# Kernel optimization log

Hardware: AMD Instinct MI355X
Metric: run time of the kernel (lower is better)

The kernel has to match this reference:

```python
import jax, jax.numpy as jnp
import numpy as np

NEG_SLOPE = 0.2

def gat_conv(x, src, dst, W, a_src, a_dst, b, heads, out_ch, num_nodes):
    # Linear projection per head: [N, H, C]
    h = (x @ W).reshape(num_nodes, heads, out_ch)
    # Per-node attention logits: [N, H]
    s_src = jnp.sum(h * a_src[None, :, :], axis=-1)
    s_dst = jnp.sum(h * a_dst[None, :, :], axis=-1)
    # Per-edge attention score, LeakyReLU(0.2): [E, H]
    e = jax.nn.leaky_relu(s_src[src] + s_dst[dst], negative_slope=NEG_SLOPE)
    # Segment softmax over incoming edges of each destination node
    e_max = jax.ops.segment_max(e, dst, num_segments=num_nodes)
    e_exp = jnp.exp(e - e_max[dst])
    denom = jax.ops.segment_sum(e_exp, dst, num_segments=num_nodes)
    alpha = e_exp / (denom[dst] + 1e-16)  # [E, H]
    # Weighted message aggregation: [N, H, C]
    msg = h[src] * alpha[:, :, None]
    out = jax.ops.segment_sum(msg, dst, num_segments=num_nodes)
    # Concat heads + bias
    return out.reshape(num_nodes, heads * out_ch) + b


def setup_inputs() -> dict:
    key = jax.random.key(0)
    ks = jax.random.split(key, 9)
    N, E = 50000, 1000000
    x = jax.random.normal(ks[0], (N, 300), dtype=jnp.float32)
    edge_index = jax.random.randint(ks[1], (2, E), 0, N, dtype=jnp.int64)
    W1 = jax.random.normal(ks[2], (300, 64), dtype=jnp.float32) * 0.05
    a_src1 = jax.random.normal(ks[3], (8, 8), dtype=jnp.float32) * 0.1
    a_dst1 = jax.random.normal(ks[4], (8, 8), dtype=jnp.float32) * 0.1
    b1 = jnp.zeros((64,), dtype=jnp.float32)
    W2 = jax.random.normal(ks[5], (64, 64), dtype=jnp.float32) * 0.1
    a_src2 = jax.random.normal(ks[6], (1, 64), dtype=jnp.float32) * 0.1
    a_dst2 = jax.random.normal(ks[7], (1, 64), dtype=jnp.float32) * 0.1
    b2 = jnp.zeros((64,), dtype=jnp.float32)
    return {"x": x, "edge_index": edge_index, "W1": W1, "a_src1": a_src1,
            "a_dst1": a_dst1, "b1": b1, "W2": W2, "a_src2": a_src2,
            "a_dst2": a_dst2, "b2": b2}


def reference(x, edge_index, W1, a_src1, a_dst1, b1, W2, a_src2, a_dst2, b2):
    N = x.shape[0]
    src, dst = edge_index[0], edge_index[1]
    # eval mode: dropouts are identity
    h = gat_conv(x, src, dst, W1, a_src1, a_dst1, b1, heads=8, out_ch=8, num_nodes=N)
    h = jax.nn.elu(h)
    out = gat_conv(h, src, dst, W2, a_src2, a_dst2, b2, heads=1, out_ch=64, num_nodes=N)
    return out
```

## Files before the change

### kernel.cpp

```cpp
#include <hip/hip_runtime.h>
#include <math.h>

#define NN 50000
#define NE 1000000
#define EC 31
#define ECP 32
#define CSH 15
#define WR 8
#define RNG 6250
#define RPAD 6272
#define NCNT (EC * WR)
#define NPB 24
#define NGB 782
#define NSB 196

typedef __bf16 bf16x8 __attribute__((ext_vector_type(8)));
typedef float f32x4 __attribute__((ext_vector_type(4)));

__device__ inline unsigned short f2bf(float f) {
    unsigned u = __float_as_uint(f);
    u += 0x7FFFu + ((u >> 16) & 1u);
    return (unsigned short)(u >> 16);
}
__device__ inline float bf2f(unsigned short s) {
    return __uint_as_float(((unsigned)s) << 16);
}
__device__ inline float bflo(unsigned r) { return __uint_as_float(r << 16); }
__device__ inline float bfhi(unsigned r) { return __uint_as_float(r & 0xffff0000u); }
__device__ inline unsigned cvtpk(float lo, float hi) {
    unsigned u;
    asm("v_cvt_pk_bf16_f32 %0, %1, %2" : "=v"(u) : "v"(lo), "v"(hi));
    return u;
}

__global__ __launch_bounds__(1024) void k_count_prep(
        const int* __restrict__ ei, int* __restrict__ cnt,
        unsigned char* __restrict__ pos,
        const float* __restrict__ W1, const float* __restrict__ W2,
        unsigned short* __restrict__ Bt1, unsigned short* __restrict__ Bt2)
{
    __shared__ __align__(16) int sm[RNG];
    const int tid = threadIdx.x;
    const int bid = blockIdx.x;

    if (bid >= NCNT) {
        int t = (bid - NCNT) * 1024 + tid;
        if (t < 64 * 320) {
            int c = t / 320, k = t % 320;
            Bt1[t] = (k < 300) ? f2bf(W1[k * 64 + c]) : (unsigned short)0;
        } else {
            int i = t - 64 * 320;
            int c = i >> 6, k = i & 63;
            Bt2[i] = f2bf(W2[k * 64 + c]);
        }
        return;
    }
    const int c = bid >> 3, w = bid & 7;
    const int lo = w * RNG;
    for (int j = tid; j < RNG; j += 1024) sm[j] = 0;
    __syncthreads();
    const int base = c << CSH;
    #pragma unroll
    for (int it = 0; it < (1 << CSH) / 4096; ++it) {
        int e = base + (it * 1024 + tid) * 4;
        if (e < NE) {
            int4 d = *(const int4*)(ei + NE + e);
            unsigned t0 = (unsigned)(d.x - lo), t1 = (unsigned)(d.y - lo);
            unsigned t2 = (unsigned)(d.z - lo), t3 = (unsigned)(d.w - lo);
            if (t0 < RNG) pos[e]     = (unsigned char)atomicAdd(&sm[t0], 1);
            if (t1 < RNG) pos[e + 1] = (unsigned char)atomicAdd(&sm[t1], 1);
            if (t2 < RNG) pos[e + 2] = (unsigned char)atomicAdd(&sm[t2], 1);
            if (t3 < RNG) pos[e + 3] = (unsigned char)atomicAdd(&sm[t3], 1);
        }
    }
    __syncthreads();
    int* dstp = cnt + (size_t)bid * RPAD;
    for (int j = tid; j < RNG; j += 1024) dstp[j] = sm[j];
}

__global__ __launch_bounds__(256) void k_gemm_scan(
        const float* __restrict__ A, const unsigned short* __restrict__ Bt,
        unsigned short* __restrict__ hb,
        const float* __restrict__ asrc, const float* __restrict__ adst,
        float* __restrict__ ss, float* __restrict__ sd,
        const int* __restrict__ cnt, int* __restrict__ excl,
        int* __restrict__ sums, unsigned char* __restrict__ rpre)
{
    __shared__ __align__(16) unsigned short lds[9216];
    const int tid = threadIdx.x;
    const int bid = blockIdx.x;

    if (bid >= NGB) {
        const int sb = bid - NGB;
        int i = sb * 256 + tid;
        int v = 0;
        if (i < NN) {
            int w8 = i / RNG;
            int j = i - w8 * RNG;
            int run = 0;
            unsigned pk[ECP / 4];
            #pragma unroll
            for (int q = 0; q < ECP / 4; ++q) pk[q] = 0;
            #pragma unroll
            for (int cc = 0; cc < EC; ++cc) {
                pk[cc >> 2] |= ((unsigned)run & 0xffu) << ((cc & 3) * 8);
                run += cnt[(size_t)(cc * 8 + w8) * RPAD + j];
            }
            v = run;
            *(uint4*)(rpre + (size_t)i * ECP)      = make_uint4(pk[0], pk[1], pk[2], pk[3]);
            *(uint4*)(rpre + (size_t)i * ECP + 16) = make_uint4(pk[4], pk[5], pk[6], pk[7]);
        }
        int* buf = (int*)lds;
        buf[tid] = v;
        __syncthreads();
        #pragma unroll
        for (int off = 1; off < 256; off <<= 1) {
            int t = (tid >= off) ? buf[tid - off] : 0;
            __syncthreads();
            buf[tid] += t;
            __syncthreads();
        }
        if (i < NN) excl[i] = buf[tid] - v;
        if (tid == 255) sums[sb] = buf[255];
        return;
    }

    const int row0 = bid * 64;
    const int lane = tid & 63, w = tid >> 6;
    const int quad = lane >> 4, mm = lane & 15;
    const int sr = tid >> 2, q16 = (tid & 3) * 16;
    const int gsr = row0 + sr;
    const int K = 300, M = NN;

    f32x4 acc[4];
    #pragma unroll
    for (int i = 0; i < 4; ++i) acc[i] = (f32x4){0.f, 0.f, 0.f, 0.f};

    for (int kt = 0; kt < 5; ++kt) {
        const int k0 = kt * 64;
        int4 a0 = {0, 0, 0, 0}, a1 = {0, 0, 0, 0};
        if (gsr < M) {
            const float* ap = A + (size_t)gsr * K + k0 + q16;
            if (k0 + q16 + 15 < K) {
                float4 v0 = *(const float4*)ap;
                float4 v1 = *(const float4*)(ap + 4);
                float4 v2 = *(const float4*)(ap + 8);
                float4 v3 = *(const float4*)(ap + 12);
                a0.x = (int)cvtpk(v0.x, v0.y); a0.y = (int)cvtpk(v0.z, v0.w);
                a0.z = (int)cvtpk(v1.x, v1.y); a0.w = (int)cvtpk(v1.z, v1.w);
                a1.x = (int)cvtpk(v2.x, v2.y); a1.y = (int)cvtpk(v2.z, v2.w);
                a1.z = (int)cvtpk(v3.x, v3.y); a1.w = (int)cvtpk(v3.z, v3.w);
            } else {
                unsigned short* u0 = (unsigned short*)&a0;
                unsigned short* u1 = (unsigned short*)&a1;
                #pragma unroll
                for (int j = 0; j < 8; ++j)
                    u0[j] = (k0 + q16 + j < K) ? f2bf(ap[j]) : (unsigned short)0;
                #pragma unroll
                for (int j = 0; j < 8; ++j)
                    u1[j] = (k0 + q16 + 8 + j < K) ? f2bf(ap[8 + j]) : (unsigned short)0;
            }
        }
        *(int4*)(lds + sr * 72 + q16)     = a0;
        *(int4*)(lds + sr * 72 + q16 + 8) = a1;
        *(int4*)(lds + 4608 + sr * 72 + q16) =
            *(const int4*)(Bt + (size_t)sr * 320 + k0 + q16);
        *(int4*)(lds + 4608 + sr * 72 + q16 + 8) =
            *(const int4*)(Bt + (size_t)sr * 320 + k0 + q16 + 8);
        __syncthreads();
        bf16x8 af0 = *(const bf16x8*)(lds + (w * 16 + mm) * 72 + quad * 8);
        bf16x8 af1 = *(const bf16x8*)(lds + (w * 16 + mm) * 72 + 32 + quad * 8);
        #pragma unroll
        for (int nt = 0; nt < 4; ++nt) {
            bf16x8 b0 = *(const bf16x8*)(lds + 4608 + (nt * 16 + mm) * 72 + quad * 8);
            bf16x8 b1 = *(const bf16x8*)(lds + 4608 + (nt * 16 + mm) * 72 + 32 + quad * 8);
            acc[nt] = __builtin_amdgcn_mfma_f32_16x16x32_bf16(af0, b0, acc[nt], 0, 0, 0);
            acc[nt] = __builtin_amdgcn_mfma_f32_16x16x32_bf16(af1, b1, acc[nt], 0, 0, 0);
        }
        __syncthreads();
    }
    #pragma unroll
    for (int nt = 0; nt < 4; ++nt)
        #pragma unroll
        for (int reg = 0; reg < 4; ++reg)
            lds[w * 1152 + (quad * 4 + reg) * 72 + nt * 16 + mm] = f2bf(acc[nt][reg]);
    __syncthreads();
    const int cg = (tid & 3) * 16;
    const unsigned short* crow = lds + (sr >> 4) * 1152 + (sr & 15) * 72;
    if (gsr < M) {
        *(int4*)(hb + (size_t)gsr * 64 + cg)     = *(const int4*)(crow + cg);
        *(int4*)(hb + (size_t)gsr * 64 + cg + 8) = *(const int4*)(crow + cg + 8);
    }
    #pragma unroll
    for (int hh = 0; hh < 2; ++hh) {
        int hd = (tid & 3) + hh * 4;
        float pss = 0.f, psd = 0.f;
        #pragma unroll
        for (int c = 0; c < 8; ++c) {
            float hv = bf2f(crow[hd * 8 + c]);
            pss += hv * asrc[hd * 8 + c];
            psd += hv * adst[hd * 8 + c];
        }
        if (gsr < M) { ss[gsr * 8 + hd] = pss; sd[gsr * 8 + hd] = psd; }
    }
}

__global__ __launch_bounds__(256) void gemm_l2(const unsigned short* __restrict__ A,
        const unsigned short* __restrict__ Bt, unsigned short* __restrict__ hb,
        const float* __restrict__ asrc, const float* __restrict__ adst,
        float* __restrict__ ss, float* __restrict__ sd)
{
    __shared__ __align__(16) unsigned short lds[9216];
    const int tid  = threadIdx.x;
    const int row0 = blockIdx.x * 64;
    const int lane = tid & 63, w = tid >> 6;
    const int quad = lane >> 4, mm = lane & 15;
    const int sr = tid >> 2, q16 = (tid & 3) * 16;
    const int gsr = row0 + sr;

    f32x4 acc[4];
    #pragma unroll
    for (int i = 0; i < 4; ++i) acc[i] = (f32x4){0.f, 0.f, 0.f, 0.f};

    int4 a0 = {0, 0, 0, 0}, a1 = {0, 0, 0, 0};
    if (gsr < NN) {
        a0 = *(const int4*)(A + (size_t)gsr * 64 + q16);
        a1 = *(const int4*)(A + (size_t)gsr * 64 + q16 + 8);
    }
    *(int4*)(lds + sr * 72 + q16)     = a0;
    *(int4*)(lds + sr * 72 + q16 + 8) = a1;
    *(int4*)(lds + 4608 + sr * 72 + q16)     = *(const int4*)(Bt + sr * 64 + q16);
    *(int4*)(lds + 4608 + sr * 72 + q16 + 8) = *(const int4*)(Bt + sr * 64 + q16 + 8);
    __syncthreads();
    bf16x8 af0 = *(const bf16x8*)(lds + (w * 16 + mm) * 72 + quad * 8);
    bf16x8 af1 = *(const bf16x8*)(lds + (w * 16 + mm) * 72 + 32 + quad * 8);
    #pragma unroll
    for (int nt = 0; nt < 4; ++nt) {
        bf16x8 b0 = *(const bf16x8*)(lds + 4608 + (nt * 16 + mm) * 72 + quad * 8);
        bf16x8 b1 = *(const bf16x8*)(lds + 4608 + (nt * 16 + mm) * 72 + 32 + quad * 8);
        acc[nt] = __builtin_amdgcn_mfma_f32_16x16x32_bf16(af0, b0, acc[nt], 0, 0, 0);
        acc[nt] = __builtin_amdgcn_mfma_f32_16x16x32_bf16(af1, b1, acc[nt], 0, 0, 0);
    }
    __syncthreads();
    #pragma unroll
    for (int nt = 0; nt < 4; ++nt)
        #pragma unroll
        for (int reg = 0; reg < 4; ++reg)
            lds[w * 1152 + (quad * 4 + reg) * 72 + nt * 16 + mm] = f2bf(acc[nt][reg]);
    __syncthreads();
    const int cg = (tid & 3) * 16;
    const unsigned short* crow = lds + (sr >> 4) * 1152 + (sr & 15) * 72;
    if (gsr < NN) {
        *(int4*)(hb + (size_t)gsr * 64 + cg)     = *(const int4*)(crow + cg);
        *(int4*)(hb + (size_t)gsr * 64 + cg + 8) = *(const int4*)(crow + cg + 8);
    }
    int p = tid & 3;
    float pss = 0.f, psd = 0.f;
    #pragma unroll
    for (int c = 0; c < 16; ++c) {
        float hv = bf2f(crow[p * 16 + c]);
        pss += hv * asrc[p * 16 + c];
        psd += hv * adst[p * 16 + c];
    }
    pss += __shfl_xor(pss, 1); psd += __shfl_xor(psd, 1);
    pss += __shfl_xor(pss, 2); psd += __shfl_xor(psd, 2);
    if (p == 0 && gsr < NN) { ss[gsr] = pss; sd[gsr] = psd; }
}

__global__ __launch_bounds__(1024) void scan23(const int* __restrict__ excl,
        const int* __restrict__ sums, int* __restrict__ rowptr)
{
    int blk = (int)blockIdx.x * 4;
    int off = 0;
    for (int j = 0; j < blk; ++j) off += sums[j];
    int sub = (threadIdx.x >> 8);
    for (int j = 0; j < sub; ++j) off += sums[blk + j];
    int i = (int)blockIdx.x * 1024 + threadIdx.x;
    if (i < NN) rowptr[i] = excl[i] + off;
    if (i == 0) rowptr[NN] = NE;
}

__global__ __launch_bounds__(256) void scatter_k(const int* __restrict__ ei,
        const int* __restrict__ rowptr, const unsigned char* __restrict__ pos,
        const unsigned char* __restrict__ rpre, unsigned short* __restrict__ col)
{
    int e = (blockIdx.x * 256 + threadIdx.x) * 4;
    if (e >= NE) return;
    int c = e >> CSH;
    int4 s = *(const int4*)(ei + e);
    int4 d = *(const int4*)(ei + NE + e);
    uchar4 p = *(const uchar4*)(pos + e);
    int r0 = rowptr[d.x] + (int)rpre[(d.x << 5) + c] + p.x;
    int r1 = rowptr[d.y] + (int)rpre[(d.y << 5) + c] + p.y;
    int r2 = rowptr[d.z] + (int)rpre[(d.z << 5) + c] + p.z;
    int r3 = rowptr[d.w] + (int)rpre[(d.w << 5) + c] + p.w;
    col[r0] = (unsigned short)s.x;
    col[r1] = (unsigned short)s.y;
    col[r2] = (unsigned short)s.z;
    col[r3] = (unsigned short)s.w;
}

#define LEAKY(s) ((s) > 0.f ? (s) : 0.2f * (s))

__global__ __launch_bounds__(256) void agg_l1(const int* __restrict__ rowptr,
        const unsigned short* __restrict__ col, const unsigned short* __restrict__ hb,
        const float* __restrict__ ss, const float* __restrict__ sd,
        const float* __restrict__ b, unsigned short* __restrict__ out)
{
    int n = (blockIdx.x * 256 + threadIdx.x) >> 6;
    int lane = threadIdx.x & 63;
    if (n >= NN) return;
    const int es = lane >> 4;
    const int cg = (lane & 15) << 2;
    const int hd = cg >> 3;
    float sdst = sd[n * 8 + hd];
    int r0 = rowptr[n], r1 = rowptr[n + 1];
    f32x4 acc = {0.f, 0.f, 0.f, 0.f};
    float dsum = 0.f;
    for (int i = r0; i < r1; i += 32) {
        int av[8]; bool vv[8];
        #pragma unroll
        for (int u = 0; u < 8; ++u) {
            int e = i + u * 4 + es;
            vv[u] = e < r1;
            av[u] = (int)col[vv[u] ? e : r0];
        }
        uint2 rr[8]; float sv[8];
        #pragma unroll
        for (int u = 0; u < 8; ++u) {
            rr[u] = *(const uint2*)(hb + av[u] * 64 + cg);
            sv[u] = ss[av[u] * 8 + hd];
        }
        #pragma unroll
        for (int u = 0; u < 8; ++u) {
            float wv = vv[u] ? __expf(LEAKY(sv[u] + sdst)) : 0.f;
            acc[0] += wv * bflo(rr[u].x);
            acc[1] += wv * bfhi(rr[u].x);
            acc[2] += wv * bflo(rr[u].y);
            acc[3] += wv * bfhi(rr[u].y);
            dsum += wv;
        }
    }
    #pragma unroll
    for (int m = 16; m <= 32; m <<= 1) {
        acc[0] += __shfl_xor(acc[0], m); acc[1] += __shfl_xor(acc[1], m);
        acc[2] += __shfl_xor(acc[2], m); acc[3] += __shfl_xor(acc[3], m);
        dsum += __shfl_xor(dsum, m);
    }
    if (es == 0) {
        float inv = 1.f / (dsum + 1e-16f);
        float v0 = acc[0] * inv + b[cg + 0]; v0 = v0 > 0.f ? v0 : __expf(v0) - 1.f;
        float v1 = acc[1] * inv + b[cg + 1]; v1 = v1 > 0.f ? v1 : __expf(v1) - 1.f;
        float v2 = acc[2] * inv + b[cg + 2]; v2 = v2 > 0.f ? v2 : __expf(v2) - 1.f;
        float v3 = acc[3] * inv + b[cg + 3]; v3 = v3 > 0.f ? v3 : __expf(v3) - 1.f;
        unsigned o01 = (unsigned)f2bf(v0) | ((unsigned)f2bf(v1) << 16);
        unsigned o23 = (unsigned)f2bf(v2) | ((unsigned)f2bf(v3) << 16);
        *(uint2*)(out + n * 64 + cg) = make_uint2(o01, o23);
    }
}

__global__ __launch_bounds__(256) void agg_l2(const int* __restrict__ rowptr,
        const unsigned short* __restrict__ col, const unsigned short* __restrict__ hb,
        const float* __restrict__ ss, const float* __restrict__ sd,
        const float* __restrict__ b, float* __restrict__ out)
{
    int n = (blockIdx.x * 256 + threadIdx.x) >> 6;
    int lane = threadIdx.x & 63;
    if (n >= NN) return;
    const int es = lane >> 4;
    const int cg = (lane & 15) << 2;
    float sdst = sd[n];
    int r0 = rowptr[n], r1 = rowptr[n + 1];
    f32x4 acc = {0.f, 0.f, 0.f, 0.f};
    float dsum = 0.f;
    for (int i = r0; i < r1; i += 32) {
        int av[8]; bool vv[8];
        #pragma unroll
        for (int u = 0; u < 8; ++u) {
            int e = i + u * 4 + es;
            vv[u] = e < r1;
            av[u] = (int)col[vv[u] ? e : r0];
        }
        uint2 rr[8]; float sv[8];
        #pragma unroll
        for (int u = 0; u < 8; ++u) {
            rr[u] = *(const uint2*)(hb + av[u] * 64 + cg);
            sv[u] = ss[av[u]];
        }
        #pragma unroll
        for (int u = 0; u < 8; ++u) {
            float wv = vv[u] ? __expf(LEAKY(sv[u] + sdst)) : 0.f;
            acc[0] += wv * bflo(rr[u].x);
            acc[1] += wv * bfhi(rr[u].x);
            acc[2] += wv * bflo(rr[u].y);
            acc[3] += wv * bfhi(rr[u].y);
            dsum += wv;
        }
    }
    #pragma unroll
    for (int m = 16; m <= 32; m <<= 1) {
        acc[0] += __shfl_xor(acc[0], m); acc[1] += __shfl_xor(acc[1], m);
        acc[2] += __shfl_xor(acc[2], m); acc[3] += __shfl_xor(acc[3], m);
        dsum += __shfl_xor(dsum, m);
    }
    if (es == 0) {
        float inv = 1.f / (dsum + 1e-16f);
        float4 o;
        o.x = acc[0] * inv + b[cg + 0];
        o.y = acc[1] * inv + b[cg + 1];
        o.z = acc[2] * inv + b[cg + 2];
        o.w = acc[3] * inv + b[cg + 3];
        *(float4*)(out + n * 64 + cg) = o;
    }
}

extern "C" void kernel_launch(void* const* d_in, const int* in_sizes, int n_in,
                              void* d_out, int out_size, void* d_ws, size_t ws_size,
                              hipStream_t stream)
{
    const float* x      = (const float*)d_in[0];
    const int*   ei     = (const int*)d_in[1];
    const float* W1     = (const float*)d_in[2];
    const float* a_src1 = (const float*)d_in[3];
    const float* a_dst1 = (const float*)d_in[4];
    const float* b1     = (const float*)d_in[5];
    const float* W2     = (const float*)d_in[6];
    const float* a_src2 = (const float*)d_in[7];
    const float* a_dst2 = (const float*)d_in[8];
    const float* b2     = (const float*)d_in[9];
    float* out = (float*)d_out;

    char* wp = (char*)d_ws;
    unsigned short* hb  = (unsigned short*)wp;  wp += (size_t)NN * 64 * 2;
    unsigned short* P1b = (unsigned short*)wp;  wp += (size_t)NN * 64 * 2;
    unsigned short* Bt1 = (unsigned short*)wp;  wp += (size_t)64 * 320 * 2;
    unsigned short* Bt2 = (unsigned short*)wp;  wp += (size_t)64 * 64 * 2;
    float* ss1 = (float*)wp;  wp += (size_t)NN * 8 * 4;
    float* sd1 = (float*)wp;  wp += (size_t)NN * 8 * 4;
    int* cnt    = (int*)wp;  wp += (size_t)NCNT * RPAD * 4;
    unsigned char* rpre = (unsigned char*)wp;  wp += (size_t)NN * ECP;
    int* excl   = (int*)wp;  wp += (size_t)NN * 4;
    int* sums   = (int*)wp;  wp += 256 * 4;
    int* rowptr = (int*)wp;  wp += (size_t)(NN + 4) * 4;
    unsigned short* col = (unsigned short*)wp;  wp += (size_t)(NE + 8) * 2;
    unsigned char*  pos = (unsigned char*)wp;   wp += (size_t)NE;
    float* ss2 = ss1;
    float* sd2 = ss1 + NN;

    const int NB = (NN + 1023) / 1024;

    k_count_prep<<<NCNT + NPB, 1024, 0, stream>>>(ei, cnt, pos, W1, W2, Bt1, Bt2);
    k_gemm_scan<<<NGB + NSB, 256, 0, stream>>>(
        x, Bt1, hb, a_src1, a_dst1, ss1, sd1, cnt, excl, sums, rpre);
    scan23<<<NB, 1024, 0, stream>>>(excl, sums, rowptr);
    scatter_k<<<(NE / 4 + 255) / 256, 256, 0, stream>>>(ei, rowptr, pos, rpre, col);

    agg_l1<<<(NN * 64 + 255) / 256, 256, 0, stream>>>(rowptr, col, hb, ss1, sd1, b1, P1b);
    gemm_l2<<<(NN + 63) / 64, 256, 0, stream>>>(P1b, Bt2, hb, a_src2, a_dst2, ss2, sd2);
    agg_l2<<<(NN * 64 + 255) / 256, 256, 0, stream>>>(rowptr, col, hb, ss2, sd2, b2, out);
}
```

Baseline: 218.0 us.

## Map each destination node to 32 lanes instead of a full wave in aggregation

Both GAT aggregation kernels now assign a half-wave (32 lanes) per destination node, processing 16 edges per iteration instead of 32, and the launch grids are halved. With an average in-degree near 20, this cuts idle lanes and the padded gathers that come from oversizing the edge loop. The trade-off is more loop iterations per node, and two nodes with different degrees now share one wave, so they can diverge.

```diff
diff --git a/kernel.cpp b/kernel.cpp
--- a/kernel.cpp
+++ b/kernel.cpp
@@ -307,21 +307,21 @@
         const float* __restrict__ ss, const float* __restrict__ sd,
         const float* __restrict__ b, unsigned short* __restrict__ out)
 {
-    int n = (blockIdx.x * 256 + threadIdx.x) >> 6;
-    int lane = threadIdx.x & 63;
+    int n = (blockIdx.x * 256 + threadIdx.x) >> 5;
+    int lane32 = threadIdx.x & 31;
     if (n >= NN) return;
-    const int es = lane >> 4;
-    const int cg = (lane & 15) << 2;
+    const int es = lane32 >> 4;
+    const int cg = (lane32 & 15) << 2;
     const int hd = cg >> 3;
     float sdst = sd[n * 8 + hd];
     int r0 = rowptr[n], r1 = rowptr[n + 1];
     f32x4 acc = {0.f, 0.f, 0.f, 0.f};
     float dsum = 0.f;
-    for (int i = r0; i < r1; i += 32) {
+    for (int i = r0; i < r1; i += 16) {
         int av[8]; bool vv[8];
         #pragma unroll
         for (int u = 0; u < 8; ++u) {
-            int e = i + u * 4 + es;
+            int e = i + u * 2 + es;
             vv[u] = e < r1;
             av[u] = (int)col[vv[u] ? e : r0];
         }
@@ -341,12 +341,9 @@
             dsum += wv;
         }
     }
-    #pragma unroll
-    for (int m = 16; m <= 32; m <<= 1) {
-        acc[0] += __shfl_xor(acc[0], m); acc[1] += __shfl_xor(acc[1], m);
-        acc[2] += __shfl_xor(acc[2], m); acc[3] += __shfl_xor(acc[3], m);
-        dsum += __shfl_xor(dsum, m);
-    }
+    acc[0] += __shfl_xor(acc[0], 16); acc[1] += __shfl_xor(acc[1], 16);
+    acc[2] += __shfl_xor(acc[2], 16); acc[3] += __shfl_xor(acc[3], 16);
+    dsum += __shfl_xor(dsum, 16);
     if (es == 0) {
         float inv = 1.f / (dsum + 1e-16f);
         float v0 = acc[0] * inv + b[cg + 0]; v0 = v0 > 0.f ? v0 : __expf(v0) - 1.f;
@@ -364,20 +361,20 @@
         const float* __restrict__ ss, const float* __restrict__ sd,
         const float* __restrict__ b, float* __restrict__ out)
 {
-    int n = (blockIdx.x * 256 + threadIdx.x) >> 6;
-    int lane = threadIdx.x & 63;
+    int n = (blockIdx.x * 256 + threadIdx.x) >> 5;
+    int lane32 = threadIdx.x & 31;
     if (n >= NN) return;
-    const int es = lane >> 4;
-    const int cg = (lane & 15) << 2;
+    const int es = lane32 >> 4;
+    const int cg = (lane32 & 15) << 2;
     float sdst = sd[n];
     int r0 = rowptr[n], r1 = rowptr[n + 1];
     f32x4 acc = {0.f, 0.f, 0.f, 0.f};
     float dsum = 0.f;
-    for (int i = r0; i < r1; i += 32) {
+    for (int i = r0; i < r1; i += 16) {
         int av[8]; bool vv[8];
         #pragma unroll
         for (int u = 0; u < 8; ++u) {
-            int e = i + u * 4 + es;
+            int e = i + u * 2 + es;
             vv[u] = e < r1;
             av[u] = (int)col[vv[u] ? e : r0];
         }
@@ -397,12 +394,9 @@
             dsum += wv;
         }
     }
-    #pragma unroll
-    for (int m = 16; m <= 32; m <<= 1) {
-        acc[0] += __shfl_xor(acc[0], m); acc[1] += __shfl_xor(acc[1], m);
-        acc[2] += __shfl_xor(acc[2], m); acc[3] += __shfl_xor(acc[3], m);
-        dsum += __shfl_xor(dsum, m);
-    }
+    acc[0] += __shfl_xor(acc[0], 16); acc[1] += __shfl_xor(acc[1], 16);
+    acc[2] += __shfl_xor(acc[2], 16); acc[3] += __shfl_xor(acc[3], 16);
+    dsum += __shfl_xor(dsum, 16);
     if (es == 0) {
         float inv = 1.f / (dsum + 1e-16f);
         float4 o;
@@ -455,7 +449,7 @@
     scan23<<<NB, 1024, 0, stream>>>(excl, sums, rowptr);
     scatter_k<<<(NE / 4 + 255) / 256, 256, 0, stream>>>(ei, rowptr, pos, rpre, col);
 
-    agg_l1<<<(NN * 64 + 255) / 256, 256, 0, stream>>>(rowptr, col, hb, ss1, sd1, b1, P1b);
+    agg_l1<<<(NN * 32 + 255) / 256, 256, 0, stream>>>(rowptr, col, hb, ss1, sd1, b1, P1b);
     gemm_l2<<<(NN + 63) / 64, 256, 0, stream>>>(P1b, Bt2, hb, a_src2, a_dst2, ss2, sd2);
-    agg_l2<<<(NN * 64 + 255) / 256, 256, 0, stream>>>(rowptr, col, hb, ss2, sd2, b2, out);
-}
+    agg_l2<<<(NN * 32 + 255) / 256, 256, 0, stream>>>(rowptr, col, hb, ss2, sd2, b2, out);
+}
```

Result: no change. 220.0 us (+0.9%).
